# Performance work log

Measured on AMD Instinct MI355X. Metric: run time of the kernel, lower is better.

Reference implementation:

```python
import jax, jax.numpy as jnp
import numpy as np

H = 64  # lstm_units
FORGET_BIAS = 1.0  # TF LSTMCell default


def setup_inputs() -> dict:
    key = jax.random.key(0)
    k1, k2, k3 = jax.random.split(key, 3)
    B, T = 256, 2048
    x = jax.random.normal(k1, (B, T, 1), dtype=jnp.float32)
    # Layer 1: LSTMCell(64), input dim 1 -> kernel [(1+64), 4*64]
    W1 = jax.random.normal(k2, (1 + H, 4 * H), dtype=jnp.float32) * 0.1
    b1 = jnp.zeros((4 * H,), dtype=jnp.float32)
    # Layer 2: LSTMCell(1), input dim 64 -> kernel [(64+1), 4*1]
    W2 = jax.random.normal(k3, (H + 1, 4), dtype=jnp.float32) * 0.1
    b2 = jnp.zeros((4,), dtype=jnp.float32)
    return {"x": x, "W1": W1, "b1": b1, "W2": W2, "b2": b2}


def _lstm_step(c, h, xt, W, b):
    # TF LSTMCell: gates from concat([x, h]) @ W + b, order i, j, f, o
    z = jnp.concatenate([xt, h], axis=-1) @ W + b
    i, j, f, o = jnp.split(z, 4, axis=-1)
    c_new = jax.nn.sigmoid(f + FORGET_BIAS) * c + jax.nn.sigmoid(i) * jnp.tanh(j)
    h_new = jax.nn.sigmoid(o) * jnpp_tanh(c_new) if False else jax.nn.sigmoid(o) * jnp.tanh(c_new)
    return c_new, h_new


def reference(x, W1, b1, W2, b2):
    # x: [B, T, 1] -> outputs of 2-layer stacked LSTM, final layer size 1
    B = x.shape[0]

    def step(carry, xt):
        c1, h1, c2, h2 = carry
        c1, h1 = _lstm_step(c1, h1, xt, W1, b1)
        c2, h2 = _lstm_step(c2, h2, h1, W2, b2)
        return (c1, h1, c2, h2), h2

    init = (
        jnp.zeros((B, H), x.dtype),
        jnp.zeros((B, H), x.dtype),
        jnp.zeros((B, 1), x.dtype),
        jnp.zeros((B, 1), x.dtype),
    )
    x_tbf = jnp.swapaxes(x, 0, 1)  # [T, B, 1]
    _, ys = jax.lax.scan(step, init, x_tbf)  # ys: [T, B, 1]
    return jnp.swapaxes(ys, 0, 1)  # [B, T, 1]
```

## Files before the change

kernel.cpp:

```cpp
#include <hip/hip_runtime.h>

constexpr int kT = 2048;
constexpr int kB = 256;
constexpr int kH = 64;

__device__ __forceinline__ float fast_sig(float x) {
    return __builtin_amdgcn_rcpf(1.0f + __expf(-x));
}
__device__ __forceinline__ float fast_tanh(float x) {
    float t = __expf(2.0f * x);
    return 1.0f - 2.0f * __builtin_amdgcn_rcpf(t + 1.0f);
}

__global__ __launch_bounds__(320) void lstm2_kernel(
    const float* __restrict__ x, const float* __restrict__ W1,
    const float* __restrict__ b1, const float* __restrict__ W2,
    const float* __restrict__ b2, float* __restrict__ out)
{
    __shared__ float x_lds[kT];
    __shared__ float h1_lds[2][kH];
    __shared__ float a_lds[4 * kH];

    const int tid = threadIdx.x;
    const int b = blockIdx.x;
    const float* xg = x + (size_t)b * kT;
    float* outg = out + (size_t)b * kT;

    for (int i = tid; i < kT; i += 320) x_lds[i] = xg[i];
    if (tid < kH) { h1_lds[0][tid] = 0.0f; h1_lds[1][tid] = 0.0f; }

    float w0 = 0.0f, b1g = 0.0f;
    float wh[kH];
    float c1 = 0.0f;
    float4 w2u = {0, 0, 0, 0}, w2t = {0, 0, 0, 0}, b2v = {0, 0, 0, 0};
    float c2 = 0.0f, h2 = 0.0f;

    if (tid < 256) {
        w0  = W1[tid];
        b1g = b1[tid];
        #pragma unroll
        for (int k = 0; k < kH; ++k) wh[k] = W1[(k + 1) * 256 + tid];
    } else {
        const int u = tid - 256;
        w2u = ((const float4*)W2)[u];
        w2t = ((const float4*)W2)[kH];
        b2v = ((const float4*)b2)[0];
    }
    __syncthreads();

    int cur = 0;
    for (int t = 0; t < kT; ++t) {
        const int nxt = cur ^ 1;
        if (tid < 256) {
            float z = fmaf(x_lds[t], w0, b1g);
            const float4* h4 = (const float4*)h1_lds[cur];
            #pragma unroll
            for (int k = 0; k < kH / 4; ++k) {
                float4 h = h4[k];
                z = fmaf(h.x, wh[4 * k + 0], z);
                z = fmaf(h.y, wh[4 * k + 1], z);
                z = fmaf(h.z, wh[4 * k + 2], z);
                z = fmaf(h.w, wh[4 * k + 3], z);
            }
            const int gate = tid >> 6;
            float a;
            if (gate == 1)      a = fast_tanh(z);
            else if (gate == 2) a = fast_sig(z + 1.0f);
            else                a = fast_sig(z);
            a_lds[tid] = a;
        } else if (t > 0) {
            const int u = tid - 256;
            const float hv = h1_lds[cur][u];
            float p0 = hv * w2u.x, p1 = hv * w2u.y, p2 = hv * w2u.z, p3 = hv * w2u.w;
            #pragma unroll
            for (int m = 1; m < 64; m <<= 1) {
                p0 += __shfl_xor(p0, m);
                p1 += __shfl_xor(p1, m);
                p2 += __shfl_xor(p2, m);
                p3 += __shfl_xor(p3, m);
            }
            const float zi = p0 + h2 * w2t.x + b2v.x;
            const float zj = p1 + h2 * w2t.y + b2v.y;
            const float zf = p2 + h2 * w2t.z + b2v.z;
            const float zo = p3 + h2 * w2t.w + b2v.w;
            c2 = fast_sig(zf + 1.0f) * c2 + fast_sig(zi) * fast_tanh(zj);
            h2 = fast_sig(zo) * fast_tanh(c2);
            if (u == 0) outg[t - 1] = h2;
        }
        __syncthreads();
        if ((tid >> 6) == 2) {
            const int u = tid & 63;
            const float ai = a_lds[u];
            const float aj = a_lds[64 + u];
            const float af = a_lds[128 + u];
            const float ao = a_lds[192 + u];
            c1 = fmaf(af, c1, ai * aj);
            h1_lds[nxt][u] = ao * fast_tanh(c1);
        }
        __syncthreads();
        cur = nxt;
    }

    if (tid >= 256) {
        const int u = tid - 256;
        const float hv = h1_lds[cur][u];
        float p0 = hv * w2u.x, p1 = hv * w2u.y, p2 = hv * w2u.z, p3 = hv * w2u.w;
        #pragma unroll
        for (int m = 1; m < 64; m <<= 1) {
            p0 += __shfl_xor(p0, m);
            p1 += __shfl_xor(p1, m);
            p2 += __shfl_xor(p2, m);
            p3 += __shfl_xor(p3, m);
        }
        const float zi = p0 + h2 * w2t.x + b2v.x;
        const float zj = p1 + h2 * w2t.y + b2v.y;
        const float zf = p2 + h2 * w2t.z + b2v.z;
        const float zo = p3 + h2 * w2t.w + b2v.w;
        c2 = fast_sig(zf + 1.0f) * c2 + fast_sig(zi) * fast_tanh(zj);
        h2 = fast_sig(zo) * fast_tanh(c2);
        if (u == 0) outg[kT - 1] = h2;
    }
}

extern "C" void kernel_launch(void* const* d_in, const int* in_sizes, int n_in,
                              void* d_out, int out_size, void* d_ws, size_t ws_size,
                              hipStream_t stream) {
    const float* x  = (const float*)d_in[0];
    const float* W1 = (const float*)d_in[1];
    const float* b1 = (const float*)d_in[2];
    const float* W2 = (const float*)d_in[3];
    const float* b2 = (const float*)d_in[4];
    float* out = (float*)d_out;
    lstm2_kernel<<<kB, 320, 0, stream>>>(x, W1, b1, W2, b2, out);
}
```

Baseline: 1.231 ms.

## Remap gates so each wave owns all four gates, removing a block barrier

Each of the four layer-1 waves now computes all four gates for 16 hidden units, so the gate-to-cell combine happens inside the wave through shuffles instead of a shared-memory round trip. That removes one __syncthreads per timestep and the a_lds buffer. The layer-2 work is split into two pipelined stages: a reduction of h1 one step, then the cell update on the next step, using a 16-lane reduction instead of a full 64-lane butterfly. The dot product uses four independent accumulators and tanh is computed through a sigmoid, trading a little extra arithmetic and register use for a shorter per-step critical path.

```diff
diff --git a/kernel.cpp b/kernel.cpp
--- a/kernel.cpp
+++ b/kernel.cpp
@@ -19,7 +19,6 @@
 {
     __shared__ float x_lds[kT];
     __shared__ float h1_lds[2][kH];
-    __shared__ float a_lds[4 * kH];
 
     const int tid = threadIdx.x;
     const int b = blockIdx.x;
@@ -29,20 +28,33 @@
     for (int i = tid; i < kT; i += 320) x_lds[i] = xg[i];
     if (tid < kH) { h1_lds[0][tid] = 0.0f; h1_lds[1][tid] = 0.0f; }
 
+    const int w = tid >> 6;
+    const int l = tid & 63;
+
     float w0 = 0.0f, b1g = 0.0f;
     float wh[kH];
     float c1 = 0.0f;
-    float4 w2u = {0, 0, 0, 0}, w2t = {0, 0, 0, 0}, b2v = {0, 0, 0, 0};
+    int u = 0, g = 0;
+
+    float w2p0 = 0, w2p1 = 0, w2p2 = 0, w2p3 = 0;
+    float4 w2t = {0, 0, 0, 0}, b2v = {0, 0, 0, 0};
     float c2 = 0.0f, h2 = 0.0f;
+    float zi_s = 0, zj_s = 0, zf_s = 0, zo_s = 0;
 
-    if (tid < 256) {
-        w0  = W1[tid];
-        b1g = b1[tid];
+    if (w < 4) {
+        g = l >> 4;
+        u = 16 * w + (l & 15);
+        const int col = g * 64 + u;
+        w0 = W1[col];
+        b1g = b1[col];
         #pragma unroll
-        for (int k = 0; k < kH; ++k) wh[k] = W1[(k + 1) * 256 + tid];
+        for (int k = 0; k < kH; ++k) wh[k] = W1[(k + 1) * 256 + col];
     } else {
-        const int u = tid - 256;
-        w2u = ((const float4*)W2)[u];
+        const int s = l & 15, gg = l >> 4;
+        w2p0 = W2[(s +  0) * 4 + gg];
+        w2p1 = W2[(s + 16) * 4 + gg];
+        w2p2 = W2[(s + 32) * 4 + gg];
+        w2p3 = W2[(s + 48) * 4 + gg];
         w2t = ((const float4*)W2)[kH];
         b2v = ((const float4*)b2)[0];
     }
@@ -51,74 +63,90 @@
     int cur = 0;
     for (int t = 0; t < kT; ++t) {
         const int nxt = cur ^ 1;
-        if (tid < 256) {
-            float z = fmaf(x_lds[t], w0, b1g);
+        if (w < 4) {
+            const float xt = x_lds[t];
+            float z0 = fmaf(xt, w0, b1g), z1 = 0.0f, z2 = 0.0f, z3 = 0.0f;
             const float4* h4 = (const float4*)h1_lds[cur];
             #pragma unroll
-            for (int k = 0; k < kH / 4; ++k) {
+            for (int k = 0; k < 16; ++k) {
                 float4 h = h4[k];
-                z = fmaf(h.x, wh[4 * k + 0], z);
-                z = fmaf(h.y, wh[4 * k + 1], z);
-                z = fmaf(h.z, wh[4 * k + 2], z);
-                z = fmaf(h.w, wh[4 * k + 3], z);
+                z0 = fmaf(h.x, wh[4 * k + 0], z0);
+                z1 = fmaf(h.y, wh[4 * k + 1], z1);
+                z2 = fmaf(h.z, wh[4 * k + 2], z2);
+                z3 = fmaf(h.w, wh[4 * k + 3], z3);
             }
-            const int gate = tid >> 6;
-            float a;
-            if (gate == 1)      a = fast_tanh(z);
-            else if (gate == 2) a = fast_sig(z + 1.0f);
-            else                a = fast_sig(z);
-            a_lds[tid] = a;
-        } else if (t > 0) {
-            const int u = tid - 256;
-            const float hv = h1_lds[cur][u];
-            float p0 = hv * w2u.x, p1 = hv * w2u.y, p2 = hv * w2u.z, p3 = hv * w2u.w;
-            #pragma unroll
-            for (int m = 1; m < 64; m <<= 1) {
-                p0 += __shfl_xor(p0, m);
-                p1 += __shfl_xor(p1, m);
-                p2 += __shfl_xor(p2, m);
-                p3 += __shfl_xor(p3, m);
+            float z = (z0 + z1) + (z2 + z3);
+            float zz = (g == 1) ? 2.0f * z : ((g == 2) ? z + 1.0f : z);
+            float sg = fast_sig(zz);
+            float a = (g == 1) ? fmaf(2.0f, sg, -1.0f) : sg;
+            const int base = l & 15;
+            const float ai = __shfl(a, base);
+            const float aj = __shfl(a, base + 16);
+            const float af = __shfl(a, base + 32);
+            const float ao = __shfl(a, base + 48);
+            c1 = fmaf(af, c1, ai * aj);
+            const float h1n = ao * fast_tanh(c1);
+            if (g == 0) h1_lds[nxt][u] = h1n;
+        } else {
+            if (t >= 2) {
+                const float zi = zi_s + h2 * w2t.x;
+                const float zj = zj_s + h2 * w2t.y;
+                const float zf = zf_s + h2 * w2t.z;
+                const float zo = zo_s + h2 * w2t.w;
+                c2 = fast_sig(zf + 1.0f) * c2 + fast_sig(zi) * fast_tanh(zj);
+                h2 = fast_sig(zo) * fast_tanh(c2);
+                if (l == 0) outg[t - 2] = h2;
             }
-            const float zi = p0 + h2 * w2t.x + b2v.x;
-            const float zj = p1 + h2 * w2t.y + b2v.y;
-            const float zf = p2 + h2 * w2t.z + b2v.z;
-            const float zo = p3 + h2 * w2t.w + b2v.w;
-            c2 = fast_sig(zf + 1.0f) * c2 + fast_sig(zi) * fast_tanh(zj);
-            h2 = fast_sig(zo) * fast_tanh(c2);
-            if (u == 0) outg[t - 1] = h2;
-        }
-        __syncthreads();
-        if ((tid >> 6) == 2) {
-            const int u = tid & 63;
-            const float ai = a_lds[u];
-            const float aj = a_lds[64 + u];
-            const float af = a_lds[128 + u];
-            const float ao = a_lds[192 + u];
-            c1 = fmaf(af, c1, ai * aj);
-            h1_lds[nxt][u] = ao * fast_tanh(c1);
+            if (t >= 1) {
+                const int s = l & 15;
+                const float* hb = h1_lds[cur];
+                float p = hb[s] * w2p0;
+                p = fmaf(hb[s + 16], w2p1, p);
+                p = fmaf(hb[s + 32], w2p2, p);
+                p = fmaf(hb[s + 48], w2p3, p);
+                p += __shfl_xor(p, 1);
+                p += __shfl_xor(p, 2);
+                p += __shfl_xor(p, 4);
+                p += __shfl_xor(p, 8);
+                zi_s = __shfl(p, s)      + b2v.x;
+                zj_s = __shfl(p, s + 16) + b2v.y;
+                zf_s = __shfl(p, s + 32) + b2v.z;
+                zo_s = __shfl(p, s + 48) + b2v.w;
+            }
         }
         __syncthreads();
         cur = nxt;
     }
 
-    if (tid >= 256) {
-        const int u = tid - 256;
-        const float hv = h1_lds[cur][u];
-        float p0 = hv * w2u.x, p1 = hv * w2u.y, p2 = hv * w2u.z, p3 = hv * w2u.w;
-        #pragma unroll
-        for (int m = 1; m < 64; m <<= 1) {
-            p0 += __shfl_xor(p0, m);
-            p1 += __shfl_xor(p1, m);
-            p2 += __shfl_xor(p2, m);
-            p3 += __shfl_xor(p3, m);
+    if (w == 4) {
+        {
+            const float zi = zi_s + h2 * w2t.x;
+            const float zj = zj_s + h2 * w2t.y;
+            const float zf = zf_s + h2 * w2t.z;
+            const float zo = zo_s + h2 * w2t.w;
+            c2 = fast_sig(zf + 1.0f) * c2 + fast_sig(zi) * fast_tanh(zj);
+            h2 = fast_sig(zo) * fast_tanh(c2);
+            if (l == 0) outg[kT - 2] = h2;
         }
-        const float zi = p0 + h2 * w2t.x + b2v.x;
-        const float zj = p1 + h2 * w2t.y + b2v.y;
-        const float zf = p2 + h2 * w2t.z + b2v.z;
-        const float zo = p3 + h2 * w2t.w + b2v.w;
-        c2 = fast_sig(zf + 1.0f) * c2 + fast_sig(zi) * fast_tanh(zj);
-        h2 = fast_sig(zo) * fast_tanh(c2);
-        if (u == 0) outg[kT - 1] = h2;
+        {
+            const int s = l & 15;
+            const float* hb = h1_lds[cur];
+            float p = hb[s] * w2p0;
+            p = fmaf(hb[s + 16], w2p1, p);
+            p = fmaf(hb[s + 32], w2p2, p);
+            p = fmaf(hb[s + 48], w2p3, p);
+            p += __shfl_xor(p, 1);
+            p += __shfl_xor(p, 2);
+            p += __shfl_xor(p, 4);
+            p += __shfl_xor(p, 8);
+            const float zi = __shfl(p, s)      + b2v.x + h2 * w2t.x;
+            const float zj = __shfl(p, s + 16) + b2v.y + h2 * w2t.y;
+            const float zf = __shfl(p, s + 32) + b2v.z + h2 * w2t.z;
+            const float zo = __shfl(p, s + 48) + b2v.w + h2 * w2t.w;
+            c2 = fast_sig(zf + 1.0f) * c2 + fast_sig(zi) * fast_tanh(zj);
+            h2 = fast_sig(zo) * fast_tanh(c2);
+            if (l == 0) outg[kT - 1] = h2;
+        }
     }
 }
 
```

New measurement: 1.134 ms. 1.09x faster.

## Replicate cell-state update in every wave and broadcast h via readlane

Applied to the files above, without the earlier changes.

Each of the five waves now recomputes the layer-1 cell update redundantly from double-buffered gate activations. The new hidden state is broadcast within the wave with readlane instead of going through LDS, which removes one of the two block barriers per timestep. Layer 2 is software-pipelined: its reduction runs one step ahead, and its outputs are buffered in LDS and written to global memory at the end. The cost is redundant transcendental work in every wave and 64 scalar readlane operations per step, which may serialize on the scalar path.

```diff
diff --git a/kernel.cpp b/kernel.cpp
--- a/kernel.cpp
+++ b/kernel.cpp
@@ -3,6 +3,7 @@
 constexpr int kT = 2048;
 constexpr int kB = 256;
 constexpr int kH = 64;
+constexpr int kThreads = 320;
 
 __device__ __forceinline__ float fast_sig(float x) {
     return __builtin_amdgcn_rcpf(1.0f + __expf(-x));
@@ -11,67 +12,134 @@
     float t = __expf(2.0f * x);
     return 1.0f - 2.0f * __builtin_amdgcn_rcpf(t + 1.0f);
 }
+__device__ __forceinline__ float rlane(float v, int k) {
+    return __int_as_float(__builtin_amdgcn_readlane(__float_as_int(v), k));
+}
 
-__global__ __launch_bounds__(320) void lstm2_kernel(
+__global__ __launch_bounds__(kThreads) void lstm2_kernel(
     const float* __restrict__ x, const float* __restrict__ W1,
     const float* __restrict__ b1, const float* __restrict__ W2,
     const float* __restrict__ b2, float* __restrict__ out)
 {
     __shared__ float x_lds[kT];
-    __shared__ float h1_lds[2][kH];
-    __shared__ float a_lds[4 * kH];
+    __shared__ float a_lds[2][4 * kH];
+    __shared__ float out_lds[kT];
 
     const int tid = threadIdx.x;
     const int b = blockIdx.x;
     const float* xg = x + (size_t)b * kT;
     float* outg = out + (size_t)b * kT;
 
-    for (int i = tid; i < kT; i += 320) x_lds[i] = xg[i];
-    if (tid < kH) { h1_lds[0][tid] = 0.0f; h1_lds[1][tid] = 0.0f; }
+    for (int i = tid; i < kT; i += kThreads) x_lds[i] = xg[i];
 
+    const int w = tid >> 6;
+    const int l = tid & 63;
+
+    float wv[kH];
     float w0 = 0.0f, b1g = 0.0f;
-    float wh[kH];
     float c1 = 0.0f;
-    float4 w2u = {0, 0, 0, 0}, w2t = {0, 0, 0, 0}, b2v = {0, 0, 0, 0};
+
+    float w2i = 0, w2j = 0, w2f = 0, w2o = 0;
+    float4 w2t = {0, 0, 0, 0}, b2v = {0, 0, 0, 0};
     float c2 = 0.0f, h2 = 0.0f;
+    float zi_s = 0, zj_s = 0, zf_s = 0, zo_s = 0;
 
-    if (tid < 256) {
-        w0  = W1[tid];
-        b1g = b1[tid];
+    if (w < 4) {
+        const int col = w * kH + l;
+        w0 = W1[col];
+        b1g = b1[col];
         #pragma unroll
-        for (int k = 0; k < kH; ++k) wh[k] = W1[(k + 1) * 256 + tid];
+        for (int k = 0; k < kH; ++k) wv[k] = W1[(k + 1) * 256 + col];
     } else {
-        const int u = tid - 256;
-        w2u = ((const float4*)W2)[u];
+        w2i = W2[l * 4 + 0];
+        w2j = W2[l * 4 + 1];
+        w2f = W2[l * 4 + 2];
+        w2o = W2[l * 4 + 3];
         w2t = ((const float4*)W2)[kH];
         b2v = ((const float4*)b2)[0];
     }
     __syncthreads();
 
-    int cur = 0;
     for (int t = 0; t < kT; ++t) {
-        const int nxt = cur ^ 1;
-        if (tid < 256) {
-            float z = fmaf(x_lds[t], w0, b1g);
-            const float4* h4 = (const float4*)h1_lds[cur];
+        const int pb = (t - 1) & 1;
+        const int cb = t & 1;
+        float h_new = 0.0f;
+        if (t > 0) {
+            const float ai = a_lds[pb][l];
+            const float aj = a_lds[pb][kH + l];
+            const float af = a_lds[pb][2 * kH + l];
+            const float ao = a_lds[pb][3 * kH + l];
+            c1 = fmaf(af, c1, ai * aj);
+            h_new = ao * fast_tanh(c1);
+        }
+        if (w < 4) {
+            float z0 = fmaf(x_lds[t], w0, b1g), z1 = 0.f, z2 = 0.f, z3 = 0.f;
             #pragma unroll
-            for (int k = 0; k < kH / 4; ++k) {
-                float4 h = h4[k];
-                z = fmaf(h.x, wh[4 * k + 0], z);
-                z = fmaf(h.y, wh[4 * k + 1], z);
-                z = fmaf(h.z, wh[4 * k + 2], z);
-                z = fmaf(h.w, wh[4 * k + 3], z);
+            for (int k = 0; k < 16; ++k) {
+                z0 = fmaf(rlane(h_new, 4 * k + 0), wv[4 * k + 0], z0);
+                z1 = fmaf(rlane(h_new, 4 * k + 1), wv[4 * k + 1], z1);
+                z2 = fmaf(rlane(h_new, 4 * k + 2), wv[4 * k + 2], z2);
+                z3 = fmaf(rlane(h_new, 4 * k + 3), wv[4 * k + 3], z3);
             }
-            const int gate = tid >> 6;
+            const float z = (z0 + z1) + (z2 + z3);
             float a;
-            if (gate == 1)      a = fast_tanh(z);
-            else if (gate == 2) a = fast_sig(z + 1.0f);
-            else                a = fast_sig(z);
-            a_lds[tid] = a;
-        } else if (t > 0) {
-            const int u = tid - 256;
-            const float hv = h1_lds[cur][u];
-            float p0 = hv * w2u.x, p1 = hv * w2u.y, p2 = hv * w2u.z, p3 = hv * w2u.w;
+            if (w == 1)      a = fast_tanh(z);
+            else if (w == 2) a = fast_sig(z + 1.0f);
+            else             a = fast_sig(z);
+            a_lds[cb][w * kH + l] = a;
+        } else {
+            if (t >= 2) {
+                const float zi = zi_s + h2 * w2t.x;
+                const float zj = zj_s + h2 * w2t.y;
+                const float zf = zf_s + h2 * w2t.z;
+                const float zo = zo_s + h2 * w2t.w;
+                c2 = fast_sig(zf + 1.0f) * c2 + fast_sig(zi) * fast_tanh(zj);
+                h2 = fast_sig(zo) * fast_tanh(c2);
+                if (l == 0) out_lds[t - 2] = h2;
+            }
+            if (t >= 1) {
+                float p0 = h_new * w2i;
+                float p1 = h_new * w2j;
+                float p2 = h_new * w2f;
+                float p3 = h_new * w2o;
+                #pragma unroll
+                for (int m = 1; m < 64; m <<= 1) {
+                    p0 += __shfl_xor(p0, m);
+                    p1 += __shfl_xor(p1, m);
+                    p2 += __shfl_xor(p2, m);
+                    p3 += __shfl_xor(p3, m);
+                }
+                zi_s = p0 + b2v.x;
+                zj_s = p1 + b2v.y;
+                zf_s = p2 + b2v.z;
+                zo_s = p3 + b2v.w;
+            }
+        }
+        __syncthreads();
+    }
+
+    if (w == 4) {
+        const int pb = (kT - 1) & 1;
+        const float ai = a_lds[pb][l];
+        const float aj = a_lds[pb][kH + l];
+        const float af = a_lds[pb][2 * kH + l];
+        const float ao = a_lds[pb][3 * kH + l];
+        c1 = fmaf(af, c1, ai * aj);
+        const float h_new = ao * fast_tanh(c1);
+        {
+            const float zi = zi_s + h2 * w2t.x;
+            const float zj = zj_s + h2 * w2t.y;
+            const float zf = zf_s + h2 * w2t.z;
+            const float zo = zo_s + h2 * w2t.w;
+            c2 = fast_sig(zf + 1.0f) * c2 + fast_sig(zi) * fast_tanh(zj);
+            h2 = fast_sig(zo) * fast_tanh(c2);
+            if (l == 0) out_lds[kT - 2] = h2;
+        }
+        {
+            float p0 = h_new * w2i;
+            float p1 = h_new * w2j;
+            float p2 = h_new * w2f;
+            float p3 = h_new * w2o;
             #pragma unroll
             for (int m = 1; m < 64; m <<= 1) {
                 p0 += __shfl_xor(p0, m);
@@ -79,47 +147,17 @@
                 p2 += __shfl_xor(p2, m);
                 p3 += __shfl_xor(p3, m);
             }
-            const float zi = p0 + h2 * w2t.x + b2v.x;
-            const float zj = p1 + h2 * w2t.y + b2v.y;
-            const float zf = p2 + h2 * w2t.z + b2v.z;
-            const float zo = p3 + h2 * w2t.w + b2v.w;
+            const float zi = p0 + b2v.x + h2 * w2t.x;
+            const float zj = p1 + b2v.y + h2 * w2t.y;
+            const float zf = p2 + b2v.z + h2 * w2t.z;
+            const float zo = p3 + b2v.w + h2 * w2t.w;
             c2 = fast_sig(zf + 1.0f) * c2 + fast_sig(zi) * fast_tanh(zj);
             h2 = fast_sig(zo) * fast_tanh(c2);
-            if (u == 0) outg[t - 1] = h2;
+            if (l == 0) out_lds[kT - 1] = h2;
         }
-        __syncthreads();
-        if ((tid >> 6) == 2) {
-            const int u = tid & 63;
-            const float ai = a_lds[u];
-            const float aj = a_lds[64 + u];
-            const float af = a_lds[128 + u];
-            const float ao = a_lds[192 + u];
-            c1 = fmaf(af, c1, ai * aj);
-            h1_lds[nxt][u] = ao * fast_tanh(c1);
-        }
-        __syncthreads();
-        cur = nxt;
     }
-
-    if (tid >= 256) {
-        const int u = tid - 256;
-        const float hv = h1_lds[cur][u];
-        float p0 = hv * w2u.x, p1 = hv * w2u.y, p2 = hv * w2u.z, p3 = hv * w2u.w;
-        #pragma unroll
-        for (int m = 1; m < 64; m <<= 1) {
-            p0 += __shfl_xor(p0, m);
-            p1 += __shfl_xor(p1, m);
-            p2 += __shfl_xor(p2, m);
-            p3 += __shfl_xor(p3, m);
-        }
-        const float zi = p0 + h2 * w2t.x + b2v.x;
-        const float zj = p1 + h2 * w2t.y + b2v.y;
-        const float zf = p2 + h2 * w2t.z + b2v.z;
-        const float zo = p3 + h2 * w2t.w + b2v.w;
-        c2 = fast_sig(zf + 1.0f) * c2 + fast_sig(zi) * fast_tanh(zj);
-        h2 = fast_sig(zo) * fast_tanh(c2);
-        if (u == 0) outg[kT - 1] = h2;
-    }
+    __syncthreads();
+    for (int i = tid; i < kT; i += kThreads) outg[i] = out_lds[i];
 }
 
 extern "C" void kernel_launch(void* const* d_in, const int* in_sizes, int n_in,
@@ -131,5 +169,5 @@
     const float* W2 = (const float*)d_in[3];
     const float* b2 = (const float*)d_in[4];
     float* out = (float*)d_out;
-    lstm2_kernel<<<kB, 320, 0, stream>>>(x, W1, b1, W2, b2, out);
+    lstm2_kernel<<<kB, kThreads, 0, stream>>>(x, W1, b1, W2, b2, out);
 }
```

Result: slower. 1.583 ms (+28.5%).
